# Optimization experiments

Hardware: AMD Instinct MI355X
Metric: run time of the kernel (lower is better)

The kernel has to match this reference:

```python
import jax, jax.numpy as jnp
import numpy as np

H = 1024

def setup_inputs() -> dict:
    key = jax.random.key(0)
    ks = jax.random.split(key, 10)
    B, T = 64, 256
    s = 1.0 / np.sqrt(H)  # torch LSTM init scale (uniform(-1/sqrt(H), 1/sqrt(H)))
    return {
        "x": jax.random.normal(ks[0], (B, T, H), jnp.float32),
        "h0": jax.random.normal(ks[1], (1, B, H), jnp.float32),
        "c0": jax.random.normal(ks[2], (1, B, H), jnp.float32),
        "dones": jax.random.randint(ks[3], (B, T), 0, 2).astype(bool),
        "W_ih": jax.random.uniform(ks[4], (4 * H, H), jnp.float32, -s, s),
        "W_hh": jax.random.uniform(ks[5], (4 * H, H), jnp.float32, -s, s),
        "b_ih": jax.random.uniform(ks[6], (4 * H,), jnp.float32, -s, s),
        "b_hh": jax.random.uniform(ks[7], (4 * H,), jnp.float32, -s, s),
    }


def reference(x, h0, c0, dones, W_ih, W_hh, b_ih, b_hh):
    # x: [B,T,H]; h0,c0: [1,B,H]; dones: [B,T] bool
    B, T, _ = x.shape
    xs = jnp.transpose(x, (1, 0, 2))          # [T,B,H]
    ds = jnp.transpose(dones, (1, 0))         # [T,B]
    # Precompute input projections for all steps in one big GEMM
    x_proj = jnp.einsum('tbh,gh->tbg', xs, W_ih) + b_ih + b_hh  # [T,B,4H]

    def step(carry, inp):
        h, c = carry                          # [B,H] each
        xp, done_t = inp                      # [B,4H], [B]
        gates = xp + h @ W_hh.T               # [B,4H]
        i, f, g, o = jnp.split(gates, 4, axis=-1)
        i = jax.nn.sigmoid(i)
        f = jax.nn.sigmoid(f)
        g = jnp.tanh(g)
        o = jax.nn.sigmoid(o)
        c_new = f * c + i * g
        h_new = o * jnp.tanh(c_new)
        # done-based reset applies AFTER emitting the step output
        mask = (~done_t)[:, None].astype(h_new.dtype)
        return (h_new * mask, c_new * mask), h_new

    (h_f, c_f), ys = jax.lax.scan(step, (h0[0], c0[0]), (x_proj, ds))
    out = jnp.tanh(jnp.transpose(ys, (1, 0, 2)))  # activation, [B,T,H]
    return out, h_f[None], c_f[None]
```

## Files before the change

### kernel.cpp

```cpp
#include <hip/hip_runtime.h>

typedef __attribute__((ext_vector_type(8))) short short8;
typedef __attribute__((ext_vector_type(4))) float f32x4;
typedef __attribute__((ext_vector_type(4))) unsigned int u32x4;
typedef unsigned long long ull;

__device__ __forceinline__ unsigned short f2bf(float f){
  union { float f; unsigned u; } v; v.f = f;
  return (unsigned short)((v.u + 0x7FFFu + ((v.u >> 16) & 1u)) >> 16);
}
__device__ __forceinline__ float bf2f(unsigned short u){
  union { unsigned u; float f; } v; v.u = ((unsigned)u) << 16; return v.f;
}
__device__ __forceinline__ float fsig(float x){ return 1.f / (1.f + __expf(-x)); }
__device__ __forceinline__ float ftanh(float x){ return 1.f - 2.f / (__expf(2.f * x) + 1.f); }

__device__ __forceinline__ void gld16(const void* g, void* l){
  __builtin_amdgcn_global_load_lds((const __attribute__((address_space(1))) void*)g,
                                   (__attribute__((address_space(3))) void*)l, 16, 0, 0);
}

__global__ __launch_bounds__(256) void cast_x_kernel(const float* __restrict__ x,
                                                     unsigned short* __restrict__ xT){
  const int row = blockIdx.x;
  const int b = row >> 8, t = row & 255;
  float4 v = ((const float4*)(x + (size_t)row * 1024))[threadIdx.x];
  ushort4 o; o.x = f2bf(v.x); o.y = f2bf(v.y); o.z = f2bf(v.z); o.w = f2bf(v.w);
  ((ushort4*)(xT + (size_t)(t * 64 + b) * 1024))[threadIdx.x] = o;
}

__global__ __launch_bounds__(256) void cast_rows_kernel(const float* __restrict__ s,
                                                        unsigned short* __restrict__ d){
  const size_t i = (size_t)blockIdx.x * 256 + threadIdx.x;
  float4 v = ((const float4*)s)[i];
  ushort4 o; o.x = f2bf(v.x); o.y = f2bf(v.y); o.z = f2bf(v.z); o.w = f2bf(v.w);
  ((ushort4*)d)[i] = o;
}

__global__ __launch_bounds__(256) void gemm_xproj_kernel(
    const unsigned short* __restrict__ A,
    const unsigned short* __restrict__ W,
    const float* __restrict__ bih,
    const float* __restrict__ bhh,
    unsigned short* __restrict__ C){
  __shared__ __align__(16) unsigned short As[2][4096];
  __shared__ __align__(16) unsigned short Bs[2][4096];
  const int tid  = threadIdx.x;
  const int lane = tid & 63;
  const int wv   = tid >> 6;
  const int wr   = wv >> 1, wc = wv & 1;
  const int mBase = blockIdx.y << 7;
  const int nBase = blockIdx.x << 7;
  const int lg4 = lane >> 4, lg15 = lane & 15;

  f32x4 acc[4][4] = {};

  auto stage = [&](int buf, int kk){
    #pragma unroll
    for (int rnd = 0; rnd < 2; ++rnd){
      const int s    = tid + (rnd << 8);
      const int row  = s >> 2;
      const int q    = s & 3;
      const int slog = q ^ (row & 3);
      const size_t col = (size_t)(kk << 5) + (slog << 3);
      unsigned short* dA = &As[buf][(size_t)((wv << 6) + (rnd << 8)) << 3];
      unsigned short* dB = &Bs[buf][(size_t)((wv << 6) + (rnd << 8)) << 3];
      gld16(A + (size_t)(mBase + row) * 1024 + col, dA);
      gld16(W + (size_t)(nBase + row) * 1024 + col, dB);
    }
  };

  stage(0, 0);
  __syncthreads();

  for (int kk = 0; kk < 32; ++kk){
    const int buf = kk & 1;
    if (kk != 31) stage(buf ^ 1, kk + 1);
    short8 af[4], bfr[4];
    #pragma unroll
    for (int mi = 0; mi < 4; ++mi){
      const int row = (wr << 6) + (mi << 4) + lg15;
      const int q   = lg4 ^ (row & 3);
      af[mi] = *(const short8*)&As[buf][(row << 5) + (q << 3)];
    }
    #pragma unroll
    for (int ni = 0; ni < 4; ++ni){
      const int row = (wc << 6) + (ni << 4) + lg15;
      const int q   = lg4 ^ (row & 3);
      bfr[ni] = *(const short8*)&Bs[buf][(row << 5) + (q << 3)];
    }
    #pragma unroll
    for (int mi = 0; mi < 4; ++mi)
      #pragma unroll
      for (int ni = 0; ni < 4; ++ni)
        acc[mi][ni] = __builtin_amdgcn_mfma_f32_16x16x32_bf16(af[mi], bfr[ni], acc[mi][ni], 0, 0, 0);
    __syncthreads();
  }

  #pragma unroll
  for (int ni = 0; ni < 4; ++ni){
    const int gcol = nBase + (wc << 6) + (ni << 4) + lg15;
    const float bsum = bih[gcol] + bhh[gcol];
    const int g = gcol >> 10, kk = gcol & 1023;
    const int ktt = kk >> 4, kc = kk & 15;
    #pragma unroll
    for (int mi = 0; mi < 4; ++mi){
      const int grow0 = mBase + (wr << 6) + (mi << 4) + (lg4 << 2);
      const int t = grow0 >> 6, b = grow0 & 63;
      const int btt = b >> 4, rb0 = b & 15;
      const size_t base = ((size_t)((t * 4 + btt) * 64 + ktt) << 10)
                          + (g << 8) + (rb0 << 4) + kc;
      #pragma unroll
      for (int r = 0; r < 4; ++r)
        C[base + (r << 4)] = f2bf(acc[mi][ni][r] + bsum);
    }
  }
}

__global__ __launch_bounds__(64, 1) void lstm_steps_kernel(
    const float* __restrict__ Whh,
    const unsigned short* __restrict__ xproj,
    const float* __restrict__ h0,
    const float* __restrict__ c0,
    const int* __restrict__ dones,
    unsigned short* __restrict__ hbuf,
    float* __restrict__ out,
    unsigned* __restrict__ bar){
  __shared__ __align__(16) unsigned short Ws[64 * 1024];
  const int lane = threadIdx.x;
  const int bt = blockIdx.x >> 6;
  const int kt = blockIdx.x & 63;
  const int b0 = bt << 4, k0 = kt << 4;
  const int l15 = lane & 15;
  const int l4  = lane >> 4;
  unsigned* cnt = bar + (bt << 6);

  {
    const int i = (kt << 6) + lane;
    const int row = i >> 8;
    const int c4 = (i & 255) << 2;
    float4 v = *(const float4*)(h0 + (size_t)(b0 + row) * 1024 + c4);
    union { ull q; unsigned short s[4]; } p;
    p.s[0] = f2bf(v.x); p.s[1] = f2bf(v.y); p.s[2] = f2bf(v.z); p.s[3] = f2bf(v.w);
    __hip_atomic_store((ull*)hbuf + (size_t)(b0 + row) * 256 + (c4 >> 2), p.q,
                       __ATOMIC_RELAXED, __HIP_MEMORY_SCOPE_AGENT);
  }
  asm volatile("s_waitcnt vmcnt(0)" ::: "memory");
  if (lane == 0)
    __hip_atomic_fetch_add(cnt, 1u, __ATOMIC_RELAXED, __HIP_MEMORY_SCOPE_AGENT);

  {
    const int wrow = lane;
    const int g = lane >> 4, j = lane & 15;
    const float* src = Whh + ((size_t)(g << 10) + k0 + j) * 1024;
    for (int c = 0; c < 1024; c += 8){
      float4 v0 = *(const float4*)(src + c);
      float4 v1 = *(const float4*)(src + c + 4);
      short8 pk;
      pk[0] = (short)f2bf(v0.x); pk[1] = (short)f2bf(v0.y);
      pk[2] = (short)f2bf(v0.z); pk[3] = (short)f2bf(v0.w);
      pk[4] = (short)f2bf(v1.x); pk[5] = (short)f2bf(v1.y);
      pk[6] = (short)f2bf(v1.z); pk[7] = (short)f2bf(v1.w);
      const int q = (c >> 3) ^ (wrow & 7);
      *(short8*)&Ws[(wrow << 10) + (q << 3)] = pk;
    }
  }

  ull pk0, pk1, pk2, pk3;
  {
    const int* dp = dones + (size_t)(b0 + l15) * 256 + (l4 << 6);
    ull w = 0;
    for (int j = 0; j < 64; ++j) w |= ((ull)(dp[j] != 0)) << j;
    pk0 = __shfl(w, l15);
    pk1 = __shfl(w, 16 + l15);
    pk2 = __shfl(w, 32 + l15);
    pk3 = __shfl(w, 48 + l15);
  }

  float creg[4];
  {
    float4 cv = *(const float4*)(c0 + (size_t)(b0 + l15) * 1024 + k0 + (l4 << 2));
    creg[0] = cv.x; creg[1] = cv.y; creg[2] = cv.z; creg[3] = cv.w;
  }

  const ull* xpb = (const ull*)xproj;
  ull xpc[4];
  {
    const size_t ch0 = ((size_t)(bt * 64 + kt)) << 8;
    #pragma unroll
    for (int g = 0; g < 4; ++g) xpc[g] = xpb[ch0 + (g << 6) + (l15 << 2) + l4];
  }

  union AV { u32x4 u4; short8 v; };

#define LDH(i, OFF) asm volatile("global_load_dwordx4 %0, %1, off offset:" OFF " sc0 sc1" \
    : "=v"(hv[i].u4) : "v"(hbase));
#define CONSUME(KB) \
  _Pragma("unroll") \
  for (int j = 0; j < 8; ++j){ \
    const int ks = ((KB) << 3) + j; \
    _Pragma("unroll") \
    for (int g = 0; g < 4; ++g){ \
      const int wrow = (g << 4) + l15; \
      const int qs = ((ks << 2) + l4) ^ (wrow & 7); \
      const short8 wf = *(const short8*)&Ws[(wrow << 10) + (qs << 3)]; \
      acc[g] = __builtin_amdgcn_mfma_f32_16x16x32_bf16(wf, hv[ks].v, acc[g], 0, 0, 0); \
    } \
  }

  #pragma unroll
  for (int qq = 0; qq < 4; ++qq){
    const ull pkq = (qq == 0) ? pk0 : (qq == 1) ? pk1 : (qq == 2) ? pk2 : pk3;
    for (int t2 = 0; t2 < 64; ++t2){
      const int t = (qq << 6) + t2;
      const ull* hc = (const ull*)hbuf + ((size_t)(t & 1) << 14);
      ull* hn = (ull*)hbuf + ((size_t)((t + 1) & 1) << 14);

      if (lane == 0){
        const unsigned tgt = ((unsigned)t + 1u) << 6;
        while (__hip_atomic_load(cnt, __ATOMIC_RELAXED, __HIP_MEMORY_SCOPE_AGENT) < tgt)
          __builtin_amdgcn_s_sleep(1);
      }
      asm volatile("" ::: "memory");

      asm volatile("s_waitcnt vmcnt(0)" ::: "memory");
      __builtin_amdgcn_sched_barrier(0);

      AV hv[32];
      const char* hbase = (const char*)hc + ((size_t)(b0 + l15) << 11) + (l4 << 4);
      LDH(0,"0")    LDH(1,"64")    LDH(2,"128")   LDH(3,"192")
      LDH(4,"256")  LDH(5,"320")   LDH(6,"384")   LDH(7,"448")
      LDH(8,"512")  LDH(9,"576")   LDH(10,"640")  LDH(11,"704")
      LDH(12,"768") LDH(13,"832")  LDH(14,"896")  LDH(15,"960")
      LDH(16,"1024") LDH(17,"1088") LDH(18,"1152") LDH(19,"1216")
      LDH(20,"1280") LDH(21,"1344") LDH(22,"1408") LDH(23,"1472")
      LDH(24,"1536") LDH(25,"1600") LDH(26,"1664") LDH(27,"1728")
      LDH(28,"1792") LDH(29,"1856") LDH(30,"1920") LDH(31,"1984")

      f32x4 acc[4];
      #pragma unroll
      for (int g = 0; g < 4; ++g){
        union { ull q; unsigned short s[4]; } u; u.q = xpc[g];
        #pragma unroll
        for (int r = 0; r < 4; ++r) acc[g][r] = bf2f(u.s[r]);
      }

      asm volatile("s_waitcnt vmcnt(24)" ::: "memory");
      __builtin_amdgcn_sched_barrier(0);
      CONSUME(0)
      asm volatile("s_waitcnt vmcnt(16)" ::: "memory");
      __builtin_amdgcn_sched_barrier(0);
      CONSUME(1)
      asm volatile("s_waitcnt vmcnt(8)" ::: "memory");
      __builtin_amdgcn_sched_barrier(0);
      CONSUME(2)
      asm volatile("s_waitcnt vmcnt(0)" ::: "memory");
      __builtin_amdgcn_sched_barrier(0);
      CONSUME(3)

      const float m = ((pkq >> t2) & 1ull) ? 0.f : 1.f;
      float ot4[4], hm4[4];
      unsigned short hb16[4];
      #pragma unroll
      for (int r = 0; r < 4; ++r){
        const float ig = fsig(acc[0][r]);
        const float fg = fsig(acc[1][r]);
        const float gg = ftanh(acc[2][r]);
        const float og = fsig(acc[3][r]);
        const float cn = fg * creg[r] + ig * gg;
        const float hv2 = og * ftanh(cn);
        ot4[r] = ftanh(hv2);
        creg[r] = cn * m;
        const float hm = hv2 * m;
        hm4[r] = hm;
        hb16[r] = f2bf(hm);
      }

      {
        union { ull q; unsigned short s[4]; } p;
        p.s[0] = hb16[0]; p.s[1] = hb16[1]; p.s[2] = hb16[2]; p.s[3] = hb16[3];
        __hip_atomic_store(hn + (size_t)(b0 + l15) * 256 + (k0 >> 2) + l4, p.q,
                           __ATOMIC_RELAXED, __HIP_MEMORY_SCOPE_AGENT);
      }
      asm volatile("s_waitcnt vmcnt(0)" ::: "memory");
      if (lane == 0)
        __hip_atomic_fetch_add(cnt, 1u, __ATOMIC_RELAXED, __HIP_MEMORY_SCOPE_AGENT);

      *(float4*)(out + (size_t)(b0 + l15) * 262144 + ((size_t)t << 10) + k0 + (l4 << 2))
          = make_float4(ot4[0], ot4[1], ot4[2], ot4[3]);
      if (t == 255){
        float* hf = out + 16777216 + (size_t)(b0 + l15) * 1024 + k0 + (l4 << 2);
        float* cf = out + 16842752 + (size_t)(b0 + l15) * 1024 + k0 + (l4 << 2);
        *(float4*)hf = make_float4(hm4[0], hm4[1], hm4[2], hm4[3]);
        *(float4*)cf = make_float4(creg[0], creg[1], creg[2], creg[3]);
      }
      {
        const int tn = (t < 255) ? t + 1 : 255;
        const size_t chn = ((size_t)((tn * 4 + bt) * 64 + kt)) << 8;
        #pragma unroll
        for (int g = 0; g < 4; ++g) xpc[g] = xpb[chn + (g << 6) + (l15 << 2) + l4];
      }
    }
  }
#undef LDH
#undef CONSUME
}

extern "C" void kernel_launch(void* const* d_in, const int* in_sizes, int n_in,
                              void* d_out, int out_size, void* d_ws, size_t ws_size,
                              hipStream_t stream){
  const float* x    = (const float*)d_in[0];
  const float* h0   = (const float*)d_in[1];
  const float* c0   = (const float*)d_in[2];
  const int*   dn   = (const int*)d_in[3];
  const float* Wih  = (const float*)d_in[4];
  const float* Whh  = (const float*)d_in[5];
  const float* bih  = (const float*)d_in[6];
  const float* bhh  = (const float*)d_in[7];
  float* out = (float*)d_out;
  char* ws = (char*)d_ws;

  unsigned short* xT    = (unsigned short*)(ws);
  unsigned short* Wib   = (unsigned short*)(ws + 33554432);
  unsigned short* xproj = (unsigned short*)(ws + 41943040);
  unsigned short* hbuf  = (unsigned short*)(ws + 176160768);
  unsigned*       bar   = (unsigned*)(ws + 176422912);

  cast_x_kernel<<<16384, 256, 0, stream>>>(x, xT);
  cast_rows_kernel<<<4096, 256, 0, stream>>>(Wih, Wib);
  gemm_xproj_kernel<<<dim3(32, 128), 256, 0, stream>>>(xT, Wib, bih, bhh, xproj);
  hipMemsetAsync(bar, 0, 1024, stream);

  const float* Whh_ = Whh; const unsigned short* xp_ = xproj;
  const float* h0_ = h0; const float* c0_ = c0; const int* dn_ = dn;
  unsigned short* hb_ = hbuf; float* out_ = out; unsigned* bar_ = bar;
  void* args[] = {&Whh_, &xp_, &h0_, &c0_, &dn_, &hb_, &out_, &bar_};
  hipError_t ce = hipLaunchCooperativeKernel((void*)lstm_steps_kernel, dim3(256), dim3(64),
                                             args, 0, stream);
  if (ce != hipSuccess){
    lstm_steps_kernel<<<256, 64, 0, stream>>>(Whh_, xp_, h0_, c0_, dn_, hb_, out_, bar_);
  }
}
```

Before: 1.705 ms.

## Replace per-step counter barrier with tagged h-data polling over a 4-slot ring

Removes the per-step atomic counter increment and spin-wait on it. Each h value now carries a tag bit in the low bit of every bf16, and is written into a 4-deep per-batch-tile ring buffer whose next slot is cleared ahead of use. Consumers load h, detect untagged (zero) chunks and re-poll only those until they arrive, so data movement doubles as synchronisation. The tag slightly perturbs the h values. The staged vmcnt overlap between h loads and MFMA consumption is lost, since everything now waits for all loads first.

```diff
diff --git a/kernel.cpp b/kernel.cpp
--- a/kernel.cpp
+++ b/kernel.cpp
@@ -8,9 +8,6 @@
 __device__ __forceinline__ unsigned short f2bf(float f){
   union { float f; unsigned u; } v; v.f = f;
   return (unsigned short)((v.u + 0x7FFFu + ((v.u >> 16) & 1u)) >> 16);
-}
-__device__ __forceinline__ float bf2f(unsigned short u){
-  union { unsigned u; float f; } v; v.u = ((unsigned)u) << 16; return v.f;
 }
 __device__ __forceinline__ float fsig(float x){ return 1.f / (1.f + __expf(-x)); }
 __device__ __forceinline__ float ftanh(float x){ return 1.f - 2.f / (__expf(2.f * x) + 1.f); }
@@ -133,16 +130,23 @@
   const int b0 = bt << 4, k0 = kt << 4;
   const int l15 = lane & 15;
   const int l4  = lane >> 4;
+  ull* hb = (ull*)hbuf + ((size_t)bt << 14);
+  const ull TAG = 0x0001000100010001ull;
+  const size_t myslice = (size_t)l15 * 256 + (kt << 2) + l4;
   unsigned* cnt = bar + (bt << 6);
 
   {
+    __hip_atomic_store(hb +           myslice, 0ull, __ATOMIC_RELAXED, __HIP_MEMORY_SCOPE_AGENT);
+    __hip_atomic_store(hb + 4096    + myslice, 0ull, __ATOMIC_RELAXED, __HIP_MEMORY_SCOPE_AGENT);
+    __hip_atomic_store(hb + 8192    + myslice, 0ull, __ATOMIC_RELAXED, __HIP_MEMORY_SCOPE_AGENT);
     const int i = (kt << 6) + lane;
     const int row = i >> 8;
     const int c4 = (i & 255) << 2;
     float4 v = *(const float4*)(h0 + (size_t)(b0 + row) * 1024 + c4);
     union { ull q; unsigned short s[4]; } p;
     p.s[0] = f2bf(v.x); p.s[1] = f2bf(v.y); p.s[2] = f2bf(v.z); p.s[3] = f2bf(v.w);
-    __hip_atomic_store((ull*)hbuf + (size_t)(b0 + row) * 256 + (c4 >> 2), p.q,
+    p.q |= TAG;
+    __hip_atomic_store(hb + 12288 + (size_t)row * 256 + (c4 >> 2), p.q,
                        __ATOMIC_RELAXED, __HIP_MEMORY_SCOPE_AGENT);
   }
   asm volatile("s_waitcnt vmcnt(0)" ::: "memory");
@@ -191,10 +195,20 @@
     for (int g = 0; g < 4; ++g) xpc[g] = xpb[ch0 + (g << 6) + (l15 << 2) + l4];
   }
 
+  if (lane == 0){
+    while (__hip_atomic_load(cnt, __ATOMIC_RELAXED, __HIP_MEMORY_SCOPE_AGENT) < 64u)
+      __builtin_amdgcn_s_sleep(1);
+  }
+  asm volatile("" ::: "memory");
+
   union AV { u32x4 u4; short8 v; };
 
 #define LDH(i, OFF) asm volatile("global_load_dwordx4 %0, %1, off offset:" OFF " sc0 sc1" \
     : "=v"(hv[i].u4) : "v"(hbase));
+#define RLDH(i, OFF) if (stale & (1u << i)) { asm volatile( \
+    "global_load_dwordx4 %0, %1, off offset:" OFF " sc0 sc1" \
+    : "=v"(hv[i].u4) : "v"(hbase)); }
+#define BAD(i) ((((hv[i].u4.x) & 0xFFFFu) * ((hv[i].u4.z) & 0xFFFFu)) == 0u)
 #define CONSUME(KB) \
   _Pragma("unroll") \
   for (int j = 0; j < 8; ++j){ \
@@ -213,21 +227,16 @@
     const ull pkq = (qq == 0) ? pk0 : (qq == 1) ? pk1 : (qq == 2) ? pk2 : pk3;
     for (int t2 = 0; t2 < 64; ++t2){
       const int t = (qq << 6) + t2;
-      const ull* hc = (const ull*)hbuf + ((size_t)(t & 1) << 14);
-      ull* hn = (ull*)hbuf + ((size_t)((t + 1) & 1) << 14);
-
-      if (lane == 0){
-        const unsigned tgt = ((unsigned)t + 1u) << 6;
-        while (__hip_atomic_load(cnt, __ATOMIC_RELAXED, __HIP_MEMORY_SCOPE_AGENT) < tgt)
-          __builtin_amdgcn_s_sleep(1);
-      }
-      asm volatile("" ::: "memory");
-
-      asm volatile("s_waitcnt vmcnt(0)" ::: "memory");
-      __builtin_amdgcn_sched_barrier(0);
+      const int bufR = (t + 3) & 3;
+      const int bufW = t & 3;
+      const int bufZ = (t + 1) & 3;
+
+      __hip_atomic_store(hb + ((size_t)bufZ << 12) + myslice, 0ull,
+                         __ATOMIC_RELAXED, __HIP_MEMORY_SCOPE_AGENT);
 
       AV hv[32];
-      const char* hbase = (const char*)hc + ((size_t)(b0 + l15) << 11) + (l4 << 4);
+      const char* hbase = (const char*)(hb + ((size_t)bufR << 12)) +
+                          ((size_t)l15 << 11) + (l4 << 4);
       LDH(0,"0")    LDH(1,"64")    LDH(2,"128")   LDH(3,"192")
       LDH(4,"256")  LDH(5,"320")   LDH(6,"384")   LDH(7,"448")
       LDH(8,"512")  LDH(9,"576")   LDH(10,"640")  LDH(11,"704")
@@ -236,27 +245,43 @@
       LDH(20,"1280") LDH(21,"1344") LDH(22,"1408") LDH(23,"1472")
       LDH(24,"1536") LDH(25,"1600") LDH(26,"1664") LDH(27,"1728")
       LDH(28,"1792") LDH(29,"1856") LDH(30,"1920") LDH(31,"1984")
+      asm volatile("s_waitcnt vmcnt(0)" ::: "memory");
+      __builtin_amdgcn_sched_barrier(0);
+
+      unsigned stale = 0;
+      #pragma unroll
+      for (int c = 0; c < 32; ++c) if (BAD(c)) stale |= (1u << c);
+      int guard = 0;
+      while (__any((int)(stale != 0u)) && ++guard < 65536){
+        RLDH(0,"0")    RLDH(1,"64")    RLDH(2,"128")   RLDH(3,"192")
+        RLDH(4,"256")  RLDH(5,"320")   RLDH(6,"384")   RLDH(7,"448")
+        RLDH(8,"512")  RLDH(9,"576")   RLDH(10,"640")  RLDH(11,"704")
+        RLDH(12,"768") RLDH(13,"832")  RLDH(14,"896")  RLDH(15,"960")
+        RLDH(16,"1024") RLDH(17,"1088") RLDH(18,"1152") RLDH(19,"1216")
+        RLDH(20,"1280") RLDH(21,"1344") RLDH(22,"1408") RLDH(23,"1472")
+        RLDH(24,"1536") RLDH(25,"1600") RLDH(26,"1664") RLDH(27,"1728")
+        RLDH(28,"1792") RLDH(29,"1856") RLDH(30,"1920") RLDH(31,"1984")
+        asm volatile("s_waitcnt vmcnt(0)" ::: "memory");
+        __builtin_amdgcn_sched_barrier(0);
+        unsigned ns = 0;
+        #pragma unroll
+        for (int c = 0; c < 32; ++c)
+          if ((stale & (1u << c)) && BAD(c)) ns |= (1u << c);
+        stale = ns;
+      }
 
       f32x4 acc[4];
       #pragma unroll
       for (int g = 0; g < 4; ++g){
         union { ull q; unsigned short s[4]; } u; u.q = xpc[g];
         #pragma unroll
-        for (int r = 0; r < 4; ++r) acc[g][r] = bf2f(u.s[r]);
-      }
-
-      asm volatile("s_waitcnt vmcnt(24)" ::: "memory");
-      __builtin_amdgcn_sched_barrier(0);
-      CONSUME(0)
-      asm volatile("s_waitcnt vmcnt(16)" ::: "memory");
-      __builtin_amdgcn_sched_barrier(0);
-      CONSUME(1)
-      asm volatile("s_waitcnt vmcnt(8)" ::: "memory");
-      __builtin_amdgcn_sched_barrier(0);
-      CONSUME(2)
-      asm volatile("s_waitcnt vmcnt(0)" ::: "memory");
-      __builtin_amdgcn_sched_barrier(0);
-      CONSUME(3)
+        for (int r = 0; r < 4; ++r){
+          union { unsigned uu; float f; } w; w.uu = ((unsigned)u.s[r]) << 16;
+          acc[g][r] = w.f;
+        }
+      }
+
+      CONSUME(0) CONSUME(1) CONSUME(2) CONSUME(3)
 
       const float m = ((pkq >> t2) & 1ull) ? 0.f : 1.f;
       float ot4[4], hm4[4];
@@ -279,12 +304,10 @@
       {
         union { ull q; unsigned short s[4]; } p;
         p.s[0] = hb16[0]; p.s[1] = hb16[1]; p.s[2] = hb16[2]; p.s[3] = hb16[3];
-        __hip_atomic_store(hn + (size_t)(b0 + l15) * 256 + (k0 >> 2) + l4, p.q,
+        p.q |= TAG;
+        __hip_atomic_store(hb + ((size_t)bufW << 12) + myslice, p.q,
                            __ATOMIC_RELAXED, __HIP_MEMORY_SCOPE_AGENT);
       }
-      asm volatile("s_waitcnt vmcnt(0)" ::: "memory");
-      if (lane == 0)
-        __hip_atomic_fetch_add(cnt, 1u, __ATOMIC_RELAXED, __HIP_MEMORY_SCOPE_AGENT);
 
       *(float4*)(out + (size_t)(b0 + l15) * 262144 + ((size_t)t << 10) + k0 + (l4 << 2))
           = make_float4(ot4[0], ot4[1], ot4[2], ot4[3]);
@@ -303,6 +326,8 @@
     }
   }
 #undef LDH
+#undef RLDH
+#undef BAD
 #undef CONSUME
 }
 
@@ -324,7 +349,7 @@
   unsigned short* Wib   = (unsigned short*)(ws + 33554432);
   unsigned short* xproj = (unsigned short*)(ws + 41943040);
   unsigned short* hbuf  = (unsigned short*)(ws + 176160768);
-  unsigned*       bar   = (unsigned*)(ws + 176422912);
+  unsigned*       bar   = (unsigned*)(ws + 176685056);
 
   cast_x_kernel<<<16384, 256, 0, stream>>>(x, xT);
   cast_rows_kernel<<<4096, 256, 0, stream>>>(Wih, Wib);
```

Measured after the change: 1.908 ms. 1.12x slower.
